# Optimization experiments

Hardware: AMD Instinct MI355X
Metric: run time of the kernel (lower is better)

## Reference

```python
import jax, jax.numpy as jnp
import numpy as np

B, S, HID = 2, 2048, 768
NH, HD = 12, 64
WINDOW_HALF = 64  # local_attention // 2
ROPE_THETA = 10000.0  # local_rope_theta (layer_id=1 -> local layer)


def setup_inputs() -> dict:
    key = jax.random.key(0)
    k1, k2, k3 = jax.random.split(key, 3)
    hidden_states = jax.random.normal(k1, (B, S, HID), dtype=jnp.float32)
    Wqkv_w = jax.random.normal(k2, (3 * HID, HID), dtype=jnp.float32) * (1.0 / np.sqrt(HID))
    Wo_w = jax.random.normal(k3, (HID, HID), dtype=jnp.float32) * (1.0 / np.sqrt(HID))
    # additive sliding-window mask: 0 inside +/-WINDOW_HALF band, finfo.min outside
    idx = jnp.arange(S)
    band = jnp.abs(idx[:, None] - idx[None, :]) <= WINDOW_HALF
    neg = jnp.finfo(jnp.float32).min
    sliding_window_mask = jnp.where(band, 0.0, neg)[None, None, :, :].astype(jnp.float32)
    position_ids = jnp.tile(jnp.arange(S, dtype=jnp.int64)[None, :], (B, 1))
    return {
        "hidden_states": hidden_states,
        "Wqkv_w": Wqkv_w,
        "Wo_w": Wo_w,
        "sliding_window_mask": sliding_window_mask,
        "position_ids": position_ids,
    }


def _rotate_half(x):
    x1, x2 = jnp.split(x, 2, axis=-1)
    return jnp.concatenate((-x2, x1), axis=-1)


def _rope_cos_sin(position_ids):
    # inv_freq: [HD//2]
    inv_freq = 1.0 / (ROPE_THETA ** (jnp.arange(0, HD, 2, dtype=jnp.float32) / HD))
    freqs = position_ids.astype(jnp.float32)[:, :, None] * inv_freq[None, None, :]  # [B,S,HD//2]
    emb = jnp.concatenate((freqs, freqs), axis=-1)  # [B,S,HD]
    return jnp.cos(emb), jnp.sin(emb)


def reference(hidden_states, Wqkv_w, Wo_w, sliding_window_mask, position_ids):
    bs, s, _ = hidden_states.shape
    qkv = hidden_states @ Wqkv_w.T  # [B,S,3*HID]
    qkv = qkv.reshape(bs, s, 3, NH, HD)
    # transpose(3,1).unbind(2) -> q,k,v each [B,NH,S,HD]
    qkv = jnp.transpose(qkv, (0, 3, 2, 1, 4))
    q, k, v = qkv[:, :, 0], qkv[:, :, 1], qkv[:, :, 2]
    cos, sin = _rope_cos_sin(position_ids)  # [B,S,HD]
    cos = cos[:, None, :, :].astype(hidden_states.dtype)
    sin = sin[:, None, :, :].astype(hidden_states.dtype)
    q = q * cos + _rotate_half(q) * sin
    k = k * cos + _rotate_half(k) * sin
    scale = 1.0 / np.sqrt(HD)
    scores = jnp.einsum("bhqd,bhkd->bhqk", q, k) * scale + sliding_window_mask
    probs = jax.nn.softmax(scores, axis=-1)
    attn = jnp.einsum("bhqk,bhkd->bhqd", probs, v)  # [B,NH,S,HD]
    attn = jnp.transpose(attn, (0, 2, 1, 3)).reshape(bs, s, NH * HD)
    return attn @ Wo_w.T
```

## Files before the change

### kernel.cpp

```cpp
#include <hip/hip_runtime.h>
#include <hip/hip_bf16.h>
#include <cstdint>

typedef __bf16 bf16_t;
typedef __bf16 bf16x8 __attribute__((ext_vector_type(8)));
typedef float f32x4 __attribute__((ext_vector_type(4)));

#define B_    2
#define S_    2048
#define HID_  768
#define NH_   12
#define HD_   64
#define KDIM_ 768

#define N_HID_  3145728
#define N_WQKV_ 1769472
#define N_WO_   589824

__device__ __forceinline__ void glds16(const bf16_t* g, const bf16_t* lds) {
  __builtin_amdgcn_global_load_lds((const __attribute__((address_space(1))) void*)g,
                                   (__attribute__((address_space(3))) void*)lds,
                                   16, 0, 0);
}

__global__ __launch_bounds__(256) void cvt3_kernel(
    const float* __restrict__ a, const float* __restrict__ b, const float* __restrict__ c,
    bf16_t* __restrict__ da, bf16_t* __restrict__ db, bf16_t* __restrict__ dc)
{
  size_t i = ((size_t)blockIdx.x * 256 + threadIdx.x) * 8;
  const float* s; bf16_t* d; size_t off;
  if (i < N_HID_)                { s = a; d = da; off = i; }
  else if (i < N_HID_ + N_WQKV_) { s = b; d = db; off = i - N_HID_; }
  else                           { s = c; d = dc; off = i - (N_HID_ + N_WQKV_); }
  float4 v0 = *(const float4*)(s + off);
  float4 v1 = *(const float4*)(s + off + 4);
  bf16x8 o;
  o[0] = (bf16_t)v0.x; o[1] = (bf16_t)v0.y; o[2] = (bf16_t)v0.z; o[3] = (bf16_t)v0.w;
  o[4] = (bf16_t)v1.x; o[5] = (bf16_t)v1.y; o[6] = (bf16_t)v1.z; o[7] = (bf16_t)v1.w;
  *(bf16x8*)(d + off) = o;
}

template<int MODE, int BM, int BN>
__launch_bounds__(256, 2)
__global__ void gemm_kernel(const bf16_t* __restrict__ A,
                            const bf16_t* __restrict__ Bw,
                            bf16_t* __restrict__ Qo,
                            bf16_t* __restrict__ Ko,
                            bf16_t* __restrict__ Vo,
                            float* __restrict__ outf)
{
  constexpr int MACC = BM / 32;
  constexpr int NWF  = BN / 32;
  constexpr int NT   = KDIM_ / 64;
  __shared__ bf16_t As[2][BM * 64];
  __shared__ bf16_t Bs[2][BN * 64];

  const int tid  = threadIdx.x;
  const int w    = tid >> 6;
  const int lane = tid & 63;
  const int wm   = w >> 1, wn = w & 1;
  const int m0   = blockIdx.y * BM;
  const int n0   = blockIdx.x * BN;
  const int lr   = lane >> 3;
  const int sub  = lane & 7;

  f32x4 acc[MACC][NWF];
#pragma unroll
  for (int i = 0; i < MACC; i++)
#pragma unroll
    for (int j = 0; j < NWF; j++) acc[i][j] = f32x4{0.f, 0.f, 0.f, 0.f};

  auto STAGE = [&](int buf, int k0) {
#pragma unroll
    for (int q = 0; q < MACC; ++q) {
      const int row = q * 32 + w * 8 + lr;
      const int c16 = sub ^ (row & 7);
      glds16(A + (size_t)(m0 + row) * KDIM_ + k0 + c16 * 8, &As[buf][(q * 32 + w * 8) * 64]);
    }
#pragma unroll
    for (int q = 0; q < NWF; ++q) {
      const int row = q * 32 + w * 8 + lr;
      const int c16 = sub ^ (row & 7);
      glds16(Bw + (size_t)(n0 + row) * KDIM_ + k0 + c16 * 8, &Bs[buf][(q * 32 + w * 8) * 64]);
    }
  };

  auto COMPUTE = [&](int buf) {
#pragma unroll
    for (int kk = 0; kk < 2; ++kk) {
      const int su = kk * 4 + (lane >> 4);
      bf16x8 af[MACC], bfr[NWF];
#pragma unroll
      for (int m = 0; m < MACC; m++) {
        const int row = wm * (BM / 2) + m * 16 + (lane & 15);
        af[m] = *(const bf16x8*)&As[buf][row * 64 + (su ^ (row & 7)) * 8];
      }
#pragma unroll
      for (int n = 0; n < NWF; n++) {
        const int row = wn * (BN / 2) + n * 16 + (lane & 15);
        bfr[n] = *(const bf16x8*)&Bs[buf][row * 64 + (su ^ (row & 7)) * 8];
      }
#pragma unroll
      for (int m = 0; m < MACC; m++)
#pragma unroll
        for (int n = 0; n < NWF; n++)
          acc[m][n] = __builtin_amdgcn_mfma_f32_16x16x32_bf16(af[m], bfr[n], acc[m][n], 0, 0, 0);
    }
  };

  STAGE(0, 0);
#pragma unroll
  for (int t = 0; t < NT; ++t) {
    if (t < NT - 1) {
      STAGE((t + 1) & 1, (t + 1) * 64);
      if constexpr (MACC + NWF == 8) asm volatile("s_waitcnt vmcnt(8)" ::: "memory");
      else                           asm volatile("s_waitcnt vmcnt(6)" ::: "memory");
    } else {
      asm volatile("s_waitcnt vmcnt(0)" ::: "memory");
    }
    __builtin_amdgcn_s_barrier();
    COMPUTE(t & 1);
    if (t < NT - 1) __builtin_amdgcn_s_barrier();
  }

  const int c = lane & 15;
  if constexpr (MODE == 1) {
#pragma unroll
    for (int m = 0; m < MACC; m++)
#pragma unroll
      for (int r = 0; r < 4; r++) {
        const int row = m0 + wm * (BM / 2) + m * 16 + (lane >> 4) * 4 + r;
#pragma unroll
        for (int nf = 0; nf < NWF; nf++)
          outf[(size_t)row * HID_ + n0 + wn * (BN / 2) + nf * 16 + c] = acc[m][nf][r];
      }
  } else {
    const int slot  = blockIdx.x * 2 + wn;
    const int which = slot / NH_;
    const int h     = slot % NH_;
    bf16_t* dst = (which == 0) ? Qo : (which == 1 ? Ko : Vo);
    const float NL = -13.287712379549449f / 32.0f;
    const float invf0 = exp2f((float)c * NL);
    const float invf1 = exp2f((float)(16 + c) * NL);
#pragma unroll
    for (int m = 0; m < MACC; m++)
#pragma unroll
      for (int r = 0; r < 4; r++) {
        const int row = m0 + wm * (BM / 2) + m * 16 + (lane >> 4) * 4 + r;
        const int b = row >> 11, s = row & 2047;
        const size_t base = ((size_t)(b * NH_ + h) * S_ + s) * HD_;
        if (which == 2) {
#pragma unroll
          for (int nf = 0; nf < 4; nf++)
            dst[base + nf * 16 + c] = (bf16_t)acc[m][nf][r];
        } else {
#pragma unroll
          for (int nf = 0; nf < 2; nf++) {
            float sn, cs;
            __sincosf((float)s * (nf ? invf1 : invf0), &sn, &cs);
            const float x1 = acc[m][nf][r], x2 = acc[m][nf + 2][r];
            dst[base + nf * 16 + c]      = (bf16_t)(x1 * cs - x2 * sn);
            dst[base + 32 + nf * 16 + c] = (bf16_t)(x2 * cs + x1 * sn);
          }
        }
      }
  }
}

__launch_bounds__(128, 4)
__global__ void attn_kernel(const bf16_t* __restrict__ Qw,
                            const bf16_t* __restrict__ Kw,
                            const bf16_t* __restrict__ Vw,
                            bf16_t* __restrict__ Ob)
{
  __shared__ bf16_t Vt[64 * 192];
  __shared__ bf16_t Pl[2][16 * 192];

  const int tid  = threadIdx.x;
  const int w    = tid >> 6;
  const int lane = tid & 63;
  const int bxq  = blockIdx.x;
  const int h    = blockIdx.y, b = blockIdx.z;
  const size_t base = (size_t)(b * NH_ + h) * S_ * HD_;
  const int kb = bxq * 32 - 64;

  const int i0 = bxq * 32 + w * 16;
  bf16x8 qf[2];
#pragma unroll
  for (int kk = 0; kk < 2; kk++)
    qf[kk] = *(const bf16x8*)(Qw + base + (size_t)(i0 + (lane & 15)) * HD_ + kk * 32 + (lane >> 4) * 8);

  {
#pragma unroll
    for (int it = 0; it < 10; ++it) {
      const int bk = it * 16 + (tid >> 3);
      const int d0 = (tid & 7) * 8;
      int j = kb + bk; j = j < 0 ? 0 : (j > S_ - 1 ? S_ - 1 : j);
      bf16x8 v = *(const bf16x8*)(Vw + base + (size_t)j * HD_ + d0);
      const int gsw = (((bk >> 3) ^ (tid & 7)) << 3) + (bk & 7);
#pragma unroll
      for (int e = 0; e < 8; e++) Vt[(d0 + e) * 192 + gsw] = v[e];
    }
    const bf16x8 z8 = {};
#pragma unroll
    for (int zz = 0; zz < 2; ++zz) {
      const int idx = zz * 128 + tid;
      const int d = idx >> 2, g = 20 + (idx & 3);
      *(bf16x8*)&Vt[d * 192 + ((g ^ (d >> 3)) << 3)] = z8;
    }
  }
  __syncthreads();

  f32x4 sc[9];
#pragma unroll
  for (int t = 0; t < 9; t++) sc[t] = f32x4{0.f, 0.f, 0.f, 0.f};
#pragma unroll
  for (int kk = 0; kk < 2; kk++) {
    const int su = kk * 4 + (lane >> 4);
#pragma unroll
    for (int t = 0; t < 9; t++) {
      const int bk = w * 16 + t * 16 + (lane & 15);
      int j = kb + bk; j = j < 0 ? 0 : (j > S_ - 1 ? S_ - 1 : j);
      bf16x8 kf = *(const bf16x8*)(Kw + base + (size_t)j * HD_ + su * 8);
      sc[t] = __builtin_amdgcn_mfma_f32_16x16x32_bf16(qf[kk], kf, sc[t], 0, 0, 0);
    }
  }

  const int c  = lane & 15;
  const int qh = lane >> 4;
  float lrow[4];
#pragma unroll
  for (int r = 0; r < 4; r++) {
    const int i = i0 + qh * 4 + r;
    float mx = -1e30f;
#pragma unroll
    for (int t = 0; t < 9; t++) {
      const int j = kb + w * 16 + t * 16 + c;
      const int dd = j - i;
      const bool valid = (dd >= -64) && (dd <= 64) && (j >= 0) && (j < S_);
      const float v = valid ? sc[t][r] * 0.125f : -1e30f;
      sc[t][r] = v;
      mx = fmaxf(mx, v);
    }
    mx = fmaxf(mx, __shfl_xor(mx, 1, 16));
    mx = fmaxf(mx, __shfl_xor(mx, 2, 16));
    mx = fmaxf(mx, __shfl_xor(mx, 4, 16));
    mx = fmaxf(mx, __shfl_xor(mx, 8, 16));
    float sum = 0.f;
#pragma unroll
    for (int t = 0; t < 9; t++) {
      const float p = __expf(sc[t][r] - mx);
      sc[t][r] = p;
      sum += p;
    }
    sum += __shfl_xor(sum, 1, 16);
    sum += __shfl_xor(sum, 2, 16);
    sum += __shfl_xor(sum, 4, 16);
    sum += __shfl_xor(sum, 8, 16);
    lrow[r] = sum;
  }

#pragma unroll
  for (int t = 0; t < 9; t++)
#pragma unroll
    for (int r = 0; r < 4; r++) {
      const int row = qh * 4 + r;
      const int col = t * 16 + c;
      Pl[w][row * 192 + (((col >> 3) ^ (row & 7)) << 3) + (col & 7)] = (bf16_t)sc[t][r];
    }
  {
    const bf16x8 z8 = {};
    const int row = lane & 15, g = 18 + ((lane >> 4) & 1);
    *(bf16x8*)&Pl[w][row * 192 + ((g ^ (row & 7)) << 3)] = z8;
  }
  asm volatile("s_waitcnt lgkmcnt(0)" ::: "memory");
  __builtin_amdgcn_sched_barrier(0);

  f32x4 ao[4];
#pragma unroll
  for (int nf = 0; nf < 4; nf++) ao[nf] = f32x4{0.f, 0.f, 0.f, 0.f};
#pragma unroll
  for (int kc = 0; kc < 5; kc++) {
    const int prow = lane & 15;
    const int Lp = kc * 32 + (lane >> 4) * 8;
    bf16x8 pf = *(const bf16x8*)&Pl[w][prow * 192 + (((Lp >> 3) ^ (prow & 7)) << 3)];
#pragma unroll
    for (int nf = 0; nf < 4; nf++) {
      const int d = nf * 16 + (lane & 15);
      const int L = w * 16 + Lp;
      bf16x8 vf = *(const bf16x8*)&Vt[d * 192 + (((L >> 3) ^ (d >> 3)) << 3)];
      ao[nf] = __builtin_amdgcn_mfma_f32_16x16x32_bf16(pf, vf, ao[nf], 0, 0, 0);
    }
  }

#pragma unroll
  for (int r = 0; r < 4; r++) {
    const float inv = 1.0f / lrow[r];
    const int srow = i0 + qh * 4 + r;
    const size_t orow = ((size_t)(b * S_ + srow)) * HID_ + h * HD_;
#pragma unroll
    for (int nf = 0; nf < 4; nf++)
      Ob[orow + nf * 16 + c] = (bf16_t)(ao[nf][r] * inv);
  }
}

extern "C" void kernel_launch(void* const* d_in, const int* in_sizes, int n_in,
                              void* d_out, int out_size, void* d_ws, size_t ws_size,
                              hipStream_t stream) {
  const float* hidden_f = (const float*)d_in[0];
  const float* wqkv_f   = (const float*)d_in[1];
  const float* wo_f     = (const float*)d_in[2];

  bf16_t* ws = (bf16_t*)d_ws;
  size_t off = 0;
  bf16_t* Hb    = ws + off; off += N_HID_;
  bf16_t* Wqkvb = ws + off; off += N_WQKV_;
  bf16_t* Wob   = ws + off; off += N_WO_;
  const size_t E = (size_t)B_ * NH_ * S_ * HD_;
  bf16_t* Q    = ws + off; off += E;
  bf16_t* K    = ws + off; off += E;
  bf16_t* V    = ws + off; off += E;
  bf16_t* ABUF = ws + off; off += E;
  float*  out  = (float*)d_out;

  cvt3_kernel<<<dim3((N_HID_ + N_WQKV_ + N_WO_) / (256 * 8)), dim3(256), 0, stream>>>(
      hidden_f, wqkv_f, wo_f, Hb, Wqkvb, Wob);
  gemm_kernel<0, 128, 128><<<dim3(18, 32), dim3(256), 0, stream>>>(Hb, Wqkvb, Q, K, V, nullptr);
  attn_kernel<<<dim3(64, 12, 2), dim3(128), 0, stream>>>(Q, K, V, ABUF);
  gemm_kernel<1, 128, 64><<<dim3(12, 32), dim3(256), 0, stream>>>(ABUF, Wob, nullptr, nullptr, nullptr, out);
}
```

Baseline: 72.46 us.

## Triple-buffer GEMM K-loop and remap blocks with XCD-aware tile swizzle

The GEMM kernel now uses three LDS stages, prefetching two K-tiles ahead with matching vmcnt waits. It also flattens the grid to 1D and remaps block IDs so consecutive tiles land on the same XCD (blockIdx & 7 chunking), which should improve L2 reuse. The output projection switches to 64x64 tiles for more blocks, and the QKV GEMM drops its min-waves hint to 1. The extra LDS stage raises shared-memory use and can lower occupancy.

```diff
diff --git a/kernel.cpp b/kernel.cpp
--- a/kernel.cpp
+++ b/kernel.cpp
@@ -21,6 +21,13 @@
   __builtin_amdgcn_global_load_lds((const __attribute__((address_space(1))) void*)g,
                                    (__attribute__((address_space(3))) void*)lds,
                                    16, 0, 0);
+}
+
+template<int N> __device__ __forceinline__ void waitvm() {
+  if constexpr (N >= 16)     asm volatile("s_waitcnt vmcnt(16)" ::: "memory");
+  else if constexpr (N == 8) asm volatile("s_waitcnt vmcnt(8)"  ::: "memory");
+  else if constexpr (N == 4) asm volatile("s_waitcnt vmcnt(4)"  ::: "memory");
+  else                       asm volatile("s_waitcnt vmcnt(0)"  ::: "memory");
 }
 
 __global__ __launch_bounds__(256) void cvt3_kernel(
@@ -40,8 +47,8 @@
   *(bf16x8*)(d + off) = o;
 }
 
-template<int MODE, int BM, int BN>
-__launch_bounds__(256, 2)
+template<int MODE, int BM, int BN, int NTX, int CHUNK, int MINW>
+__launch_bounds__(256, MINW)
 __global__ void gemm_kernel(const bf16_t* __restrict__ A,
                             const bf16_t* __restrict__ Bw,
                             bf16_t* __restrict__ Qo,
@@ -49,20 +56,24 @@
                             bf16_t* __restrict__ Vo,
                             float* __restrict__ outf)
 {
-  constexpr int MACC = BM / 32;
-  constexpr int NWF  = BN / 32;
-  constexpr int NT   = KDIM_ / 64;
-  __shared__ bf16_t As[2][BM * 64];
-  __shared__ bf16_t Bs[2][BN * 64];
+  constexpr int MACC  = BM / 32;
+  constexpr int NWF   = BN / 32;
+  constexpr int LOADS = MACC + NWF;
+  constexpr int NT    = KDIM_ / 64;
+  __shared__ bf16_t As[3][BM * 64];
+  __shared__ bf16_t Bs[3][BN * 64];
 
   const int tid  = threadIdx.x;
   const int w    = tid >> 6;
   const int lane = tid & 63;
   const int wm   = w >> 1, wn = w & 1;
-  const int m0   = blockIdx.y * BM;
-  const int n0   = blockIdx.x * BN;
-  const int lr   = lane >> 3;
-  const int sub  = lane & 7;
+  const int wk = (blockIdx.x & 7) * CHUNK + (blockIdx.x >> 3);
+  const int tx = wk % NTX;
+  const int ty = wk / NTX;
+  const int m0 = ty * BM;
+  const int n0 = tx * BN;
+  const int lr  = lane >> 3;
+  const int sub = lane & 7;
 
   f32x4 acc[MACC][NWF];
 #pragma unroll
@@ -109,17 +120,15 @@
   };
 
   STAGE(0, 0);
+  STAGE(1, 64);
 #pragma unroll
   for (int t = 0; t < NT; ++t) {
-    if (t < NT - 1) {
-      STAGE((t + 1) & 1, (t + 1) * 64);
-      if constexpr (MACC + NWF == 8) asm volatile("s_waitcnt vmcnt(8)" ::: "memory");
-      else                           asm volatile("s_waitcnt vmcnt(6)" ::: "memory");
-    } else {
-      asm volatile("s_waitcnt vmcnt(0)" ::: "memory");
-    }
+    if (t + 2 < NT) STAGE((t + 2) % 3, (t + 2) * 64);
+    if (t < NT - 2)       waitvm<2 * LOADS>();
+    else if (t == NT - 2) waitvm<LOADS>();
+    else                  waitvm<0>();
     __builtin_amdgcn_s_barrier();
-    COMPUTE(t & 1);
+    COMPUTE(t % 3);
     if (t < NT - 1) __builtin_amdgcn_s_barrier();
   }
 
@@ -135,7 +144,7 @@
           outf[(size_t)row * HID_ + n0 + wn * (BN / 2) + nf * 16 + c] = acc[m][nf][r];
       }
   } else {
-    const int slot  = blockIdx.x * 2 + wn;
+    const int slot  = tx * 2 + wn;
     const int which = slot / NH_;
     const int h     = slot % NH_;
     bf16_t* dst = (which == 0) ? Qo : (which == 1 ? Ko : Vo);
@@ -325,7 +334,7 @@
 
   cvt3_kernel<<<dim3((N_HID_ + N_WQKV_ + N_WO_) / (256 * 8)), dim3(256), 0, stream>>>(
       hidden_f, wqkv_f, wo_f, Hb, Wqkvb, Wob);
-  gemm_kernel<0, 128, 128><<<dim3(18, 32), dim3(256), 0, stream>>>(Hb, Wqkvb, Q, K, V, nullptr);
+  gemm_kernel<0, 128, 128, 18, 72, 1><<<dim3(576), dim3(256), 0, stream>>>(Hb, Wqkvb, Q, K, V, nullptr);
   attn_kernel<<<dim3(64, 12, 2), dim3(128), 0, stream>>>(Q, K, V, ABUF);
-  gemm_kernel<1, 128, 64><<<dim3(12, 32), dim3(256), 0, stream>>>(ABUF, Wob, nullptr, nullptr, nullptr, out);
-}
+  gemm_kernel<1, 64, 64, 12, 96, 2><<<dim3(768), dim3(256), 0, stream>>>(ABUF, Wob, nullptr, nullptr, nullptr, out);
+}
```

Result: slower. 79.27 us (+9.4%).
